# Performance work log

Hardware: AMD Instinct MI355X
Metric: run time of the kernel (lower is better)

The kernel has to match this reference:

```python
import jax, jax.numpy as jnp
import numpy as np

N_NODES = 100000
N_EDGES = 1600000
IN_DIM = 128
HID = 128
NUM_LAYERS = 3


def _sage_conv(h, src, dst, Wl, Wr, b, n_nodes):
    # PyG SAGEConv (aggr='mean'): out = lin_l(mean_j x_j) + lin_r(x_i)
    agg = jax.ops.segment_sum(h[src], dst, num_segments=n_nodes)
    cnt = jax.ops.segment_sum(jnp.ones((src.shape[0],), dtype=h.dtype), dst,
                              num_segments=n_nodes)
    mean = agg / jnp.maximum(cnt, 1.0)[:, None]
    return mean @ Wl + h @ Wr + b


def setup_inputs() -> dict:
    key = jax.random.key(0)
    ks = jax.random.split(key, 16)
    x = jax.random.normal(ks[0], (N_NODES, IN_DIM), dtype=jnp.float32)
    edge_index = jax.random.randint(ks[1], (2, N_EDGES), 0, N_NODES, dtype=jnp.int32)
    reranker_scores = jax.random.normal(ks[2], (N_NODES,), dtype=jnp.float32)
    inp = {"x": x, "edge_index": edge_index, "reranker_scores": reranker_scores}
    dims = [IN_DIM, HID, HID]
    for i in range(NUM_LAYERS):
        d_in = dims[i]
        s = 1.0 / np.sqrt(d_in)
        inp[f"Wl{i}"] = jax.random.uniform(ks[3 + 3 * i], (d_in, HID), jnp.float32, -s, s)
        inp[f"Wr{i}"] = jax.random.uniform(ks[4 + 3 * i], (d_in, HID), jnp.float32, -s, s)
        inp[f"b{i}"] = jax.random.uniform(ks[5 + 3 * i], (HID,), jnp.float32, -s, s)
    sh = 1.0 / np.sqrt(HID * NUM_LAYERS)
    inp["Ws"] = jax.random.uniform(ks[12], (HID * NUM_LAYERS, 1), jnp.float32, -sh, sh)
    inp["bs"] = jax.random.uniform(ks[13], (1,), jnp.float32, -sh, sh)
    inp["alpha"] = jnp.asarray(0.65, dtype=jnp.float32)
    return inp


def reference(x, edge_index, reranker_scores,
              Wl0, Wr0, b0, Wl1, Wr1, b1, Wl2, Wr2, b2,
              Ws, bs, alpha):
    src, dst = edge_index[0], edge_index[1]
    n = x.shape[0]
    params = [(Wl0, Wr0, b0), (Wl1, Wr1, b1), (Wl2, Wr2, b2)]
    xs = []
    h = x
    for (Wl, Wr, b) in params:
        h = jax.nn.relu(_sage_conv(h, src, dst, Wl, Wr, b, n))
        # dropout: eval-mode identity
        xs.append(h)
    hj = jnp.concatenate(xs, axis=-1)                 # [N, HID*NUM_LAYERS]
    gnn_scores = (hj @ Ws + bs)[:, 0]                 # [N]
    a = jax.nn.sigmoid(alpha)
    return a * reranker_scores + (1.0 - a) * gnn_scores
```

## Files before the change

### kernel.cpp

```cpp
#include <hip/hip_runtime.h>
#include <hip/hip_bf16.h>
#include <cstdint>

#define N_NODES 100000
#define HID 128
#define NBINS 391
#define CHUNK 4096

typedef __attribute__((ext_vector_type(8))) short short8v;
typedef __attribute__((ext_vector_type(4))) float floatx4;

__device__ __forceinline__ float bflo(unsigned v) { return __uint_as_float(v << 16); }
__device__ __forceinline__ float bfhi(unsigned v) { return __uint_as_float(v & 0xffff0000u); }
__device__ __forceinline__ unsigned short f2bf(float f) {
    unsigned u = __float_as_uint(f);
    unsigned r = (u + 0x7fffu + ((u >> 16) & 1u)) >> 16;
    return (unsigned short)r;
}

__global__ __launch_bounds__(256) void convx_kernel(const float* __restrict__ x,
                                                    unsigned short* __restrict__ xb, int total8) {
    int i = blockIdx.x * 256 + threadIdx.x;
    if (i >= total8) return;
    const float4* p = (const float4*)x + (size_t)i * 2;
    float4 a = p[0], b = p[1];
    uint4 o;
    o.x = f2bf(a.x) | ((unsigned)f2bf(a.y) << 16);
    o.y = f2bf(a.z) | ((unsigned)f2bf(a.w) << 16);
    o.z = f2bf(b.x) | ((unsigned)f2bf(b.y) << 16);
    o.w = f2bf(b.z) | ((unsigned)f2bf(b.w) << 16);
    *(uint4*)(xb + (size_t)i * 8) = o;
}

__global__ __launch_bounds__(256) void packw_kernel(const float* __restrict__ Wl0, const float* __restrict__ Wr0,
                                                    const float* __restrict__ Wl1, const float* __restrict__ Wr1,
                                                    const float* __restrict__ Wl2, const float* __restrict__ Wr2,
                                                    unsigned short* __restrict__ Bp) {
    int idx = blockIdx.x * 256 + threadIdx.x;
    if (idx >= 12288) return;
    int g = idx & 3, c = (idx >> 2) & 127, s = (idx >> 9) & 3, t = (idx >> 11) & 1, L = idx >> 12;
    const float* W = (t == 0) ? (L == 0 ? Wl0 : (L == 1 ? Wl1 : Wl2))
                              : (L == 0 ? Wr0 : (L == 1 ? Wr1 : Wr2));
    int k0 = s * 32 + g * 8;
    uint4 o;
    o.x = f2bf(W[(k0 + 0) * 128 + c]) | ((unsigned)f2bf(W[(k0 + 1) * 128 + c]) << 16);
    o.y = f2bf(W[(k0 + 2) * 128 + c]) | ((unsigned)f2bf(W[(k0 + 3) * 128 + c]) << 16);
    o.z = f2bf(W[(k0 + 4) * 128 + c]) | ((unsigned)f2bf(W[(k0 + 5) * 128 + c]) << 16);
    o.w = f2bf(W[(k0 + 6) * 128 + c]) | ((unsigned)f2bf(W[(k0 + 7) * 128 + c]) << 16);
    size_t chunk = (((size_t)(L * 2 + t) * 4 + s) * 128 + c) * 4 + g;
    *(uint4*)(Bp + chunk * 8) = o;
}


__global__ __launch_bounds__(256) void binhist_kernel(const int* __restrict__ dst,
                                                      int* __restrict__ cntMat, int E) {
    __shared__ int lcnt[512];
    const int tid = threadIdx.x;
    lcnt[tid] = 0; lcnt[tid + 256] = 0;
    __syncthreads();
    int base = blockIdx.x * CHUNK;
    int end = base + CHUNK; if (end > E) end = E;
    for (int i = base + tid; i < end; i += 256) atomicAdd(&lcnt[dst[i] >> 8], 1);
    __syncthreads();
    for (int j = tid; j < NBINS; j += 256) cntMat[(size_t)blockIdx.x * NBINS + j] = lcnt[j];
}

__global__ __launch_bounds__(512) void colscan_kernel(int* __restrict__ cntMat,
                                                      int* __restrict__ binCnt, int nch) {
    __shared__ int wsum[8];
    const int j = blockIdx.x;
    const int tid = threadIdx.x;
    const int lane = tid & 63, w = tid >> 6;
    int v = (tid < nch) ? cntMat[(size_t)tid * NBINS + j] : 0;
    int s = v;
    #pragma unroll
    for (int o = 1; o < 64; o <<= 1) {
        int t = __shfl_up(s, o, 64);
        if (lane >= o) s += t;
    }
    if (lane == 63) wsum[w] = s;
    __syncthreads();
    if (w == 0 && lane < 8) {
        int t = wsum[lane];
        int ss = t;
        #pragma unroll
        for (int o = 1; o < 8; o <<= 1) {
            int u = __shfl_up(ss, o, 64);
            if (lane >= o) ss += u;
        }
        wsum[lane] = ss - t;
    }
    __syncthreads();
    int excl = (s - v) + wsum[w];
    if (tid < nch) cntMat[(size_t)tid * NBINS + j] = excl;
    if (tid == 511) binCnt[j] = excl + v;
}

__global__ __launch_bounds__(512) void binbase_kernel(const int* __restrict__ binCnt,
                                                      int* __restrict__ binBase,
                                                      int* __restrict__ offs, int E) {
    __shared__ int wsum[8];
    const int tid = threadIdx.x;
    const int lane = tid & 63, w = tid >> 6;
    int v = (tid < NBINS) ? binCnt[tid] : 0;
    int s = v;
    #pragma unroll
    for (int o = 1; o < 64; o <<= 1) {
        int t = __shfl_up(s, o, 64);
        if (lane >= o) s += t;
    }
    if (lane == 63) wsum[w] = s;
    __syncthreads();
    if (w == 0 && lane < 8) {
        int t = wsum[lane];
        int ss = t;
        #pragma unroll
        for (int o = 1; o < 8; o <<= 1) {
            int u = __shfl_up(ss, o, 64);
            if (lane >= o) ss += u;
        }
        wsum[lane] = ss - t;
    }
    __syncthreads();
    if (tid < NBINS) binBase[tid] = (s - v) + wsum[w];
    if (tid == 0) offs[N_NODES] = E;
}

__global__ __launch_bounds__(256) void binscat_kernel(const int* __restrict__ src, const int* __restrict__ dst,
                                                      const int* __restrict__ cntMat,
                                                      const int* __restrict__ binBase,
                                                      unsigned* __restrict__ binned, int E) {
    __shared__ int cur[512];
    const int tid = threadIdx.x;
    const int row = blockIdx.x;
    for (int j = tid; j < NBINS; j += 256) cur[j] = cntMat[(size_t)row * NBINS + j] + binBase[j];
    __syncthreads();
    int base = row * CHUNK;
    int end = base + CHUNK; if (end > E) end = E;
    for (int i = base + tid; i < end; i += 256) {
        int d = dst[i];
        int s = src[i];
        int bin = d >> 8;
        int pos = atomicAdd(&cur[bin], 1);
        binned[pos] = (unsigned)s | ((unsigned)(d & 255) << 20);
    }
}

__global__ __launch_bounds__(256) void bincsr_kernel(const unsigned* __restrict__ binned,
                                                     const int* __restrict__ binBase, const int* __restrict__ binCnt,
                                                     int* __restrict__ esrc, int* __restrict__ offs) {
    __shared__ int h[256];
    __shared__ int cur[256];
    __shared__ int ssrc[8192];
    const int tid = threadIdx.x;
    const int bin = blockIdx.x;
    const int base = binBase[bin];
    const int cnt = binCnt[bin];
    h[tid] = 0;
    __syncthreads();
    for (int i = tid; i < cnt; i += 256) atomicAdd(&h[binned[base + i] >> 20], 1);
    __syncthreads();
    int v = h[tid];
    for (int o = 1; o < 256; o <<= 1) {
        int t = (tid >= o) ? h[tid - o] : 0;
        __syncthreads();
        h[tid] += t;
        __syncthreads();
    }
    int excl = h[tid] - v;
    cur[tid] = excl;
    int node = (bin << 8) + tid;
    if (node < N_NODES) offs[node] = base + excl;
    __syncthreads();
    for (int i = tid; i < cnt; i += 256) {
        unsigned p = binned[base + i];
        int pos = atomicAdd(&cur[p >> 20], 1);
        int s = (int)(p & 0xFFFFFu);
        if (pos < 8192) ssrc[pos] = s;
        else esrc[base + pos] = s;
    }
    __syncthreads();
    int lim = cnt < 8192 ? cnt : 8192;
    for (int i = tid; i < lim; i += 256) esrc[base + i] = ssrc[i];
}

__global__ __launch_bounds__(256) void agg_kernel(const unsigned short* __restrict__ h,
                                                  const int* __restrict__ offs,
                                                  const int* __restrict__ esrc,
                                                  unsigned short* __restrict__ mean) {
    const int lane = threadIdx.x & 63;
    const int node = blockIdx.x * 4 + (threadIdx.x >> 6);
    const int beg = offs[node], end = offs[node + 1];
    const int nb = end - beg;
    float ax = 0.f, ay = 0.f;
    for (int base = 0; base < nb; base += 64) {
        int m = nb - base; if (m > 64) m = 64;
        int sv = (lane < m) ? esrc[beg + base + lane] : 0;
        int j = 0;
        for (; j + 4 <= m; j += 4) {
            int s0 = __shfl(sv, j, 64), s1 = __shfl(sv, j + 1, 64);
            int s2 = __shfl(sv, j + 2, 64), s3 = __shfl(sv, j + 3, 64);
            unsigned v0 = *(const unsigned*)(h + (size_t)s0 * HID + lane * 2);
            unsigned v1 = *(const unsigned*)(h + (size_t)s1 * HID + lane * 2);
            unsigned v2 = *(const unsigned*)(h + (size_t)s2 * HID + lane * 2);
            unsigned v3 = *(const unsigned*)(h + (size_t)s3 * HID + lane * 2);
            ax += bflo(v0) + bflo(v1) + bflo(v2) + bflo(v3);
            ay += bfhi(v0) + bfhi(v1) + bfhi(v2) + bfhi(v3);
        }
        for (; j < m; ++j) {
            int s0 = __shfl(sv, j, 64);
            unsigned v0 = *(const unsigned*)(h + (size_t)s0 * HID + lane * 2);
            ax += bflo(v0); ay += bfhi(v0);
        }
    }
    float inv = 1.f / (float)(nb > 0 ? nb : 1);
    *(unsigned*)(mean + (size_t)node * HID + lane * 2) =
        (unsigned)f2bf(ax * inv) | ((unsigned)f2bf(ay * inv) << 16);
}

__global__ __launch_bounds__(256) void gemm_kernel(const unsigned short* __restrict__ Am,
                                                   const unsigned short* __restrict__ Ah,
                                                   const unsigned short* __restrict__ Bp,
                                                   const float* __restrict__ bias,
                                                   const float* __restrict__ Wsl,
                                                   unsigned short* __restrict__ hout,
                                                   float* __restrict__ score,
                                                   const int accum, const int writeH) {
    __shared__ unsigned short At[2 * 64 * 128];
    __shared__ float sred[2][64];
    const int tid = threadIdx.x;
    const int lane = tid & 63;
    const int w = tid >> 6;
    const int wm = w & 1, wn = w >> 1;
    const int rowBase = blockIdx.x * 64;
    const int halfRow = lane & 15;
    const int g = lane >> 4;

    {
        const unsigned short* srcs[2] = { Am, Ah };
        #pragma unroll
        for (int r = 0; r < 8; ++r) {
            int c = r * 256 + tid;
            int sIdx = c >> 10;
            int rem = c & 1023;
            int row = rem >> 4, slot = rem & 15;
            int gslot = slot ^ (row & 15);
            int grow = rowBase + row; if (grow >= N_NODES) grow = N_NODES - 1;
            const unsigned short* gp = srcs[sIdx] + (size_t)grow * HID + gslot * 8;
            unsigned ldsOff = (unsigned)(r * 4096 + w * 1024);
            __builtin_amdgcn_global_load_lds((const __attribute__((address_space(1))) void*)gp,
                                             (__attribute__((address_space(3))) void*)((char*)At + ldsOff),
                                             16, 0, 0);
        }
    }
    __syncthreads();

    floatx4 acc[2][4];
    #pragma unroll
    for (int m = 0; m < 2; m++)
        #pragma unroll
        for (int n = 0; n < 4; n++) acc[m][n] = (floatx4){0.f, 0.f, 0.f, 0.f};

    #pragma unroll
    for (int t = 0; t < 2; t++) {
        #pragma unroll
        for (int s = 0; s < 4; s++) {
            int slot = (s * 4 + g) ^ halfRow;
            int row0 = wm * 32 + halfRow;
            short8v a0 = *(const short8v*)&At[t * 8192 + row0 * 128 + slot * 8];
            short8v a1 = *(const short8v*)&At[t * 8192 + (row0 + 16) * 128 + slot * 8];
            #pragma unroll
            for (int n = 0; n < 4; n++) {
                int col = wn * 64 + n * 16 + halfRow;
                short8v b = *(const short8v*)&Bp[((((size_t)(t * 4 + s)) * 128 + col) * 4 + g) * 8];
                acc[0][n] = __builtin_amdgcn_mfma_f32_16x16x32_bf16(a0, b, acc[0][n], 0, 0, 0);
                acc[1][n] = __builtin_amdgcn_mfma_f32_16x16x32_bf16(a1, b, acc[1][n], 0, 0, 0);
            }
        }
    }

    #pragma unroll
    for (int m = 0; m < 2; m++) {
        #pragma unroll
        for (int i = 0; i < 4; i++) {
            int rloc = wm * 32 + m * 16 + g * 4 + i;
            int grow = rowBase + rloc;
            float ps = 0.f;
            #pragma unroll
            for (int n = 0; n < 4; n++) {
                int col = wn * 64 + n * 16 + halfRow;
                float v = acc[m][n][i] + bias[col];
                v = fmaxf(v, 0.f);
                if (writeH && grow < N_NODES) hout[(size_t)grow * HID + col] = f2bf(v);
                ps += v * Wsl[col];
            }
            ps += __shfl_xor(ps, 1, 64);
            ps += __shfl_xor(ps, 2, 64);
            ps += __shfl_xor(ps, 4, 64);
            ps += __shfl_xor(ps, 8, 64);
            if (halfRow == 0) sred[wn][rloc] = ps;
        }
    }
    __syncthreads();
    if (w == 0) {
        int grow = rowBase + lane;
        if (grow < N_NODES) {
            float tot = sred[0][lane] + sred[1][lane];
            score[grow] = accum ? (score[grow] + tot) : tot;
        }
    }
}

__global__ __launch_bounds__(256) void finalize_kernel(const float* __restrict__ rr, const float* __restrict__ score,
                                                       const float* __restrict__ bs, const float* __restrict__ alpha,
                                                       float* __restrict__ out, int N) {
    int i = blockIdx.x * 256 + threadIdx.x;
    if (i < N) {
        float a = 1.f / (1.f + __expf(-alpha[0]));
        out[i] = a * rr[i] + (1.f - a) * (score[i] + bs[0]);
    }
}

extern "C" void kernel_launch(void* const* d_in, const int* in_sizes, int n_in,
                              void* d_out, int out_size, void* d_ws, size_t ws_size,
                              hipStream_t stream) {
    const float* x     = (const float*)d_in[0];
    const int*   eidx  = (const int*)d_in[1];
    const float* rrs   = (const float*)d_in[2];
    const float* Wl0   = (const float*)d_in[3];
    const float* Wr0   = (const float*)d_in[4];
    const float* b0    = (const float*)d_in[5];
    const float* Wl1   = (const float*)d_in[6];
    const float* Wr1   = (const float*)d_in[7];
    const float* b1    = (const float*)d_in[8];
    const float* Wl2   = (const float*)d_in[9];
    const float* Wr2   = (const float*)d_in[10];
    const float* b2    = (const float*)d_in[11];
    const float* Ws    = (const float*)d_in[12];
    const float* bs    = (const float*)d_in[13];
    const float* alpha = (const float*)d_in[14];

    const int N = N_NODES;
    const int E = in_sizes[1] / 2;
    const int* src = eidx;
    const int* dst = eidx + E;

    uintptr_t p = (uintptr_t)d_ws;
    auto alloc = [&](size_t bytes) -> void* {
        p = (p + 255) & ~(uintptr_t)255;
        void* r = (void*)p;
        p += bytes;
        return r;
    };
    int*            offs    = (int*)alloc((size_t)(N + 1) * 4);
    int*            esrc    = (int*)alloc((size_t)E * 4);
    float*          score   = (float*)alloc((size_t)N * 4);
    int*            binBase = (int*)alloc(512 * 4);
    int*            binCnt  = (int*)alloc(512 * 4);
    unsigned short* xb      = (unsigned short*)alloc((size_t)N * HID * 2);
    unsigned short* bufA    = (unsigned short*)alloc((size_t)N * HID * 2);
    unsigned short* bufB    = (unsigned short*)alloc((size_t)N * HID * 2);
    unsigned short* Bp      = (unsigned short*)alloc((size_t)3 * 32768 * 2);

    int*      cntMat = (int*)bufA;
    unsigned* binned = (unsigned*)bufB;

    const int nch = (E + CHUNK - 1) / CHUNK;

    convx_kernel<<<6250, 256, 0, stream>>>(x, xb, N * HID / 8);
    packw_kernel<<<48, 256, 0, stream>>>(Wl0, Wr0, Wl1, Wr1, Wl2, Wr2, Bp);

    binhist_kernel<<<nch, 256, 0, stream>>>(dst, cntMat, E);
    colscan_kernel<<<NBINS, 512, 0, stream>>>(cntMat, binCnt, nch);
    binbase_kernel<<<1, 512, 0, stream>>>(binCnt, binBase, offs, E);
    binscat_kernel<<<nch, 256, 0, stream>>>(src, dst, cntMat, binBase, binned, E);
    bincsr_kernel<<<NBINS, 256, 0, stream>>>(binned, binBase, binCnt, esrc, offs);

    const int aggGrid  = N / 4;
    const int gemmGrid = (N + 63) / 64;

    agg_kernel<<<aggGrid, 256, 0, stream>>>(xb, offs, esrc, bufA);
    gemm_kernel<<<gemmGrid, 256, 0, stream>>>(bufA, xb, Bp + 0 * 32768, b0, Ws + 0 * HID, bufA, score, 0, 1);
    agg_kernel<<<aggGrid, 256, 0, stream>>>(bufA, offs, esrc, bufB);
    gemm_kernel<<<gemmGrid, 256, 0, stream>>>(bufB, bufA, Bp + 1 * 32768, b1, Ws + 1 * HID, bufB, score, 1, 1);
    agg_kernel<<<aggGrid, 256, 0, stream>>>(bufB, offs, esrc, bufA);
    gemm_kernel<<<gemmGrid, 256, 0, stream>>>(bufA, bufB, Bp + 2 * 32768, b2, Ws + 2 * HID, bufA, score, 1, 0);

    finalize_kernel<<<(N + 255) / 256, 256, 0, stream>>>(rrs, score, bs, alpha, (float*)d_out, N);
}
```

Before: 318.7 us.

## Widen agg gathers to 8-byte loads, merge prep kernels, fuse finalize into gemm

The aggregation kernel now splits each wavefront into two half-waves. Each half gathers a different neighbor row with 8-byte loads and 16 neighbors are in flight per iteration, and the halves are combined with a cross-lane shuffle at the end. This aims to increase memory-level parallelism in the gather-bound aggregation. The x conversion and weight packing kernels are merged into one launch, and the final score blend is folded into the last gemm's epilogue to save two launches and a pass over the score array. Accumulation order changes slightly, and the gather loop uses more registers.

```diff
diff --git a/kernel.cpp b/kernel.cpp
--- a/kernel.cpp
+++ b/kernel.cpp
@@ -18,37 +18,37 @@
     return (unsigned short)r;
 }
 
-__global__ __launch_bounds__(256) void convx_kernel(const float* __restrict__ x,
-                                                    unsigned short* __restrict__ xb, int total8) {
-    int i = blockIdx.x * 256 + threadIdx.x;
-    if (i >= total8) return;
-    const float4* p = (const float4*)x + (size_t)i * 2;
-    float4 a = p[0], b = p[1];
-    uint4 o;
-    o.x = f2bf(a.x) | ((unsigned)f2bf(a.y) << 16);
-    o.y = f2bf(a.z) | ((unsigned)f2bf(a.w) << 16);
-    o.z = f2bf(b.x) | ((unsigned)f2bf(b.y) << 16);
-    o.w = f2bf(b.z) | ((unsigned)f2bf(b.w) << 16);
-    *(uint4*)(xb + (size_t)i * 8) = o;
-}
-
-__global__ __launch_bounds__(256) void packw_kernel(const float* __restrict__ Wl0, const float* __restrict__ Wr0,
-                                                    const float* __restrict__ Wl1, const float* __restrict__ Wr1,
-                                                    const float* __restrict__ Wl2, const float* __restrict__ Wr2,
-                                                    unsigned short* __restrict__ Bp) {
-    int idx = blockIdx.x * 256 + threadIdx.x;
-    if (idx >= 12288) return;
-    int g = idx & 3, c = (idx >> 2) & 127, s = (idx >> 9) & 3, t = (idx >> 11) & 1, L = idx >> 12;
-    const float* W = (t == 0) ? (L == 0 ? Wl0 : (L == 1 ? Wl1 : Wl2))
-                              : (L == 0 ? Wr0 : (L == 1 ? Wr1 : Wr2));
-    int k0 = s * 32 + g * 8;
-    uint4 o;
-    o.x = f2bf(W[(k0 + 0) * 128 + c]) | ((unsigned)f2bf(W[(k0 + 1) * 128 + c]) << 16);
-    o.y = f2bf(W[(k0 + 2) * 128 + c]) | ((unsigned)f2bf(W[(k0 + 3) * 128 + c]) << 16);
-    o.z = f2bf(W[(k0 + 4) * 128 + c]) | ((unsigned)f2bf(W[(k0 + 5) * 128 + c]) << 16);
-    o.w = f2bf(W[(k0 + 6) * 128 + c]) | ((unsigned)f2bf(W[(k0 + 7) * 128 + c]) << 16);
-    size_t chunk = (((size_t)(L * 2 + t) * 4 + s) * 128 + c) * 4 + g;
-    *(uint4*)(Bp + chunk * 8) = o;
+__global__ __launch_bounds__(256) void prep_kernel(const float* __restrict__ x,
+                                                   unsigned short* __restrict__ xb, int total8,
+                                                   const float* __restrict__ Wl0, const float* __restrict__ Wr0,
+                                                   const float* __restrict__ Wl1, const float* __restrict__ Wr1,
+                                                   const float* __restrict__ Wl2, const float* __restrict__ Wr2,
+                                                   unsigned short* __restrict__ Bp) {
+    if ((int)blockIdx.x < total8 / 256) {
+        int i = blockIdx.x * 256 + threadIdx.x;
+        const float4* p = (const float4*)x + (size_t)i * 2;
+        float4 a = p[0], b = p[1];
+        uint4 o;
+        o.x = f2bf(a.x) | ((unsigned)f2bf(a.y) << 16);
+        o.y = f2bf(a.z) | ((unsigned)f2bf(a.w) << 16);
+        o.z = f2bf(b.x) | ((unsigned)f2bf(b.y) << 16);
+        o.w = f2bf(b.z) | ((unsigned)f2bf(b.w) << 16);
+        *(uint4*)(xb + (size_t)i * 8) = o;
+    } else {
+        int idx = ((int)blockIdx.x - total8 / 256) * 256 + threadIdx.x;
+        if (idx >= 12288) return;
+        int g = idx & 3, c = (idx >> 2) & 127, s = (idx >> 9) & 3, t = (idx >> 11) & 1, L = idx >> 12;
+        const float* W = (t == 0) ? (L == 0 ? Wl0 : (L == 1 ? Wl1 : Wl2))
+                                  : (L == 0 ? Wr0 : (L == 1 ? Wr1 : Wr2));
+        int k0 = s * 32 + g * 8;
+        uint4 o;
+        o.x = f2bf(W[(k0 + 0) * 128 + c]) | ((unsigned)f2bf(W[(k0 + 1) * 128 + c]) << 16);
+        o.y = f2bf(W[(k0 + 2) * 128 + c]) | ((unsigned)f2bf(W[(k0 + 3) * 128 + c]) << 16);
+        o.z = f2bf(W[(k0 + 4) * 128 + c]) | ((unsigned)f2bf(W[(k0 + 5) * 128 + c]) << 16);
+        o.w = f2bf(W[(k0 + 6) * 128 + c]) | ((unsigned)f2bf(W[(k0 + 7) * 128 + c]) << 16);
+        size_t chunk = (((size_t)(L * 2 + t) * 4 + s) * 128 + c) * 4 + g;
+        *(uint4*)(Bp + chunk * 8) = o;
+    }
 }
 
 
@@ -190,32 +190,54 @@
                                                   unsigned short* __restrict__ mean) {
     const int lane = threadIdx.x & 63;
     const int node = blockIdx.x * 4 + (threadIdx.x >> 6);
+    const int half = lane >> 5;
+    const int fl = lane & 31;
     const int beg = offs[node], end = offs[node + 1];
     const int nb = end - beg;
-    float ax = 0.f, ay = 0.f;
+    float a0 = 0.f, a1 = 0.f, a2 = 0.f, a3 = 0.f;
     for (int base = 0; base < nb; base += 64) {
         int m = nb - base; if (m > 64) m = 64;
         int sv = (lane < m) ? esrc[beg + base + lane] : 0;
         int j = 0;
-        for (; j + 4 <= m; j += 4) {
-            int s0 = __shfl(sv, j, 64), s1 = __shfl(sv, j + 1, 64);
-            int s2 = __shfl(sv, j + 2, 64), s3 = __shfl(sv, j + 3, 64);
-            unsigned v0 = *(const unsigned*)(h + (size_t)s0 * HID + lane * 2);
-            unsigned v1 = *(const unsigned*)(h + (size_t)s1 * HID + lane * 2);
-            unsigned v2 = *(const unsigned*)(h + (size_t)s2 * HID + lane * 2);
-            unsigned v3 = *(const unsigned*)(h + (size_t)s3 * HID + lane * 2);
-            ax += bflo(v0) + bflo(v1) + bflo(v2) + bflo(v3);
-            ay += bfhi(v0) + bfhi(v1) + bfhi(v2) + bfhi(v3);
-        }
-        for (; j < m; ++j) {
-            int s0 = __shfl(sv, j, 64);
-            unsigned v0 = *(const unsigned*)(h + (size_t)s0 * HID + lane * 2);
-            ax += bflo(v0); ay += bfhi(v0);
-        }
-    }
-    float inv = 1.f / (float)(nb > 0 ? nb : 1);
-    *(unsigned*)(mean + (size_t)node * HID + lane * 2) =
-        (unsigned)f2bf(ax * inv) | ((unsigned)f2bf(ay * inv) << 16);
+        for (; j + 16 <= m; j += 16) {
+            uint2 v[8];
+            #pragma unroll
+            for (int p = 0; p < 8; ++p) {
+                int s = __shfl(sv, j + 2 * p + half, 64);
+                v[p] = *(const uint2*)(h + (size_t)s * HID + fl * 4);
+            }
+            #pragma unroll
+            for (int p = 0; p < 8; ++p) {
+                a0 += bflo(v[p].x); a1 += bfhi(v[p].x);
+                a2 += bflo(v[p].y); a3 += bfhi(v[p].y);
+            }
+        }
+        for (; j + 2 <= m; j += 2) {
+            int s = __shfl(sv, j + half, 64);
+            uint2 vv = *(const uint2*)(h + (size_t)s * HID + fl * 4);
+            a0 += bflo(vv.x); a1 += bfhi(vv.x);
+            a2 += bflo(vv.y); a3 += bfhi(vv.y);
+        }
+        if (j < m) {
+            int s = __shfl(sv, j, 64);
+            if (half == 0) {
+                uint2 vv = *(const uint2*)(h + (size_t)s * HID + fl * 4);
+                a0 += bflo(vv.x); a1 += bfhi(vv.x);
+                a2 += bflo(vv.y); a3 += bfhi(vv.y);
+            }
+        }
+    }
+    a0 += __shfl_xor(a0, 32, 64);
+    a1 += __shfl_xor(a1, 32, 64);
+    a2 += __shfl_xor(a2, 32, 64);
+    a3 += __shfl_xor(a3, 32, 64);
+    if (half == 0) {
+        float inv = 1.f / (float)(nb > 0 ? nb : 1);
+        uint2 o;
+        o.x = (unsigned)f2bf(a0 * inv) | ((unsigned)f2bf(a1 * inv) << 16);
+        o.y = (unsigned)f2bf(a2 * inv) | ((unsigned)f2bf(a3 * inv) << 16);
+        *(uint2*)(mean + (size_t)node * HID + fl * 4) = o;
+    }
 }
 
 __global__ __launch_bounds__(256) void gemm_kernel(const unsigned short* __restrict__ Am,
@@ -225,7 +247,11 @@
                                                    const float* __restrict__ Wsl,
                                                    unsigned short* __restrict__ hout,
                                                    float* __restrict__ score,
-                                                   const int accum, const int writeH) {
+                                                   const float* __restrict__ rrs,
+                                                   const float* __restrict__ bsp,
+                                                   const float* __restrict__ alphap,
+                                                   float* __restrict__ outF,
+                                                   const int accum, const int writeH, const int doFinal) {
     __shared__ unsigned short At[2 * 64 * 128];
     __shared__ float sred[2][64];
     const int tid = threadIdx.x;
@@ -306,18 +332,14 @@
         int grow = rowBase + lane;
         if (grow < N_NODES) {
             float tot = sred[0][lane] + sred[1][lane];
-            score[grow] = accum ? (score[grow] + tot) : tot;
-        }
-    }
-}
-
-__global__ __launch_bounds__(256) void finalize_kernel(const float* __restrict__ rr, const float* __restrict__ score,
-                                                       const float* __restrict__ bs, const float* __restrict__ alpha,
-                                                       float* __restrict__ out, int N) {
-    int i = blockIdx.x * 256 + threadIdx.x;
-    if (i < N) {
-        float a = 1.f / (1.f + __expf(-alpha[0]));
-        out[i] = a * rr[i] + (1.f - a) * (score[i] + bs[0]);
+            if (doFinal) {
+                float sc = score[grow] + tot;
+                float a = 1.f / (1.f + __expf(-alphap[0]));
+                outF[grow] = a * rrs[grow] + (1.f - a) * (sc + bsp[0]);
+            } else {
+                score[grow] = accum ? (score[grow] + tot) : tot;
+            }
+        }
     }
 }
 
@@ -367,8 +389,8 @@
 
     const int nch = (E + CHUNK - 1) / CHUNK;
 
-    convx_kernel<<<6250, 256, 0, stream>>>(x, xb, N * HID / 8);
-    packw_kernel<<<48, 256, 0, stream>>>(Wl0, Wr0, Wl1, Wr1, Wl2, Wr2, Bp);
+    prep_kernel<<<N * HID / 8 / 256 + 48, 256, 0, stream>>>(x, xb, N * HID / 8,
+                                                            Wl0, Wr0, Wl1, Wr1, Wl2, Wr2, Bp);
 
     binhist_kernel<<<nch, 256, 0, stream>>>(dst, cntMat, E);
     colscan_kernel<<<NBINS, 512, 0, stream>>>(cntMat, binCnt, nch);
@@ -378,13 +400,15 @@
 
     const int aggGrid  = N / 4;
     const int gemmGrid = (N + 63) / 64;
+    float* outF = (float*)d_out;
 
     agg_kernel<<<aggGrid, 256, 0, stream>>>(xb, offs, esrc, bufA);
-    gemm_kernel<<<gemmGrid, 256, 0, stream>>>(bufA, xb, Bp + 0 * 32768, b0, Ws + 0 * HID, bufA, score, 0, 1);
+    gemm_kernel<<<gemmGrid, 256, 0, stream>>>(bufA, xb, Bp + 0 * 32768, b0, Ws + 0 * HID, bufA, score,
+                                              rrs, bs, alpha, outF, 0, 1, 0);
     agg_kernel<<<aggGrid, 256, 0, stream>>>(bufA, offs, esrc, bufB);
-    gemm_kernel<<<gemmGrid, 256, 0, stream>>>(bufB, bufA, Bp + 1 * 32768, b1, Ws + 1 * HID, bufB, score, 1, 1);
+    gemm_kernel<<<gemmGrid, 256, 0, stream>>>(bufB, bufA, Bp + 1 * 32768, b1, Ws + 1 * HID, bufB, score,
+                                              rrs, bs, alpha, outF, 1, 1, 0);
     agg_kernel<<<aggGrid, 256, 0, stream>>>(bufB, offs, esrc, bufA);
-    gemm_kernel<<<gemmGrid, 256, 0, stream>>>(bufA, bufB, Bp + 2 * 32768, b2, Ws + 2 * HID, bufA, score, 1, 0);
-
-    finalize_kernel<<<(N + 255) / 256, 256, 0, stream>>>(rrs, score, bs, alpha, (float*)d_out, N);
-}
+    gemm_kernel<<<gemmGrid, 256, 0, stream>>>(bufA, bufB, Bp + 2 * 32768, b2, Ws + 2 * HID, bufA, score,
+                                              rrs, bs, alpha, outF, 1, 0, 1);
+}
```

Measured after the change: 318.0 us. No clear change (-0.2%).
